# Kernel optimization log

Hardware: AMD Instinct MI355X
Metric: run time of the kernel (lower is better)

The kernel has to match this reference:

```python
import jax, jax.numpy as jnp
import numpy as np

LN_EPS = 1e-5
RMS_EPS = 1.1920929e-07  # torch.finfo(float32).eps (RMSNorm default eps=None)


def _layernorm(x, g, b):
    m = jnp.mean(x, axis=-1, keepdims=True)
    xc = x - m
    v = jnp.mean(xc * xc, axis=-1, keepdims=True)
    return xc / jnp.sqrt(v + LN_EPS) * g + b


def setup_inputs() -> dict:
    key = jax.random.key(0)
    ks = jax.random.split(key, 8)
    L, D, H, M, B, S = 4, 512, 8, 2048, 4, 2048
    std = 0.02
    return {
        "x": jax.random.normal(ks[0], (B, S, D), dtype=jnp.float32),
        # torch nn.Linear weights are [out, in]
        "Wq": jax.random.normal(ks[1], (L, D, D), dtype=jnp.float32) * std,
        "Wk": jax.random.normal(ks[2], (L, D, D), dtype=jnp.float32) * std,
        "Wv": jax.random.normal(ks[3], (L, D, D), dtype=jnp.float32) * std,
        "rms_w": jnp.ones((L, H, D // H), dtype=jnp.float32),
        "Wo": jax.random.normal(ks[4], (L, D, D), dtype=jnp.float32) * std,
        "bo": jnp.zeros((L, D), dtype=jnp.float32),
        "diffw": jnp.full((L,), 0.2, dtype=jnp.float32),
        "g_ffn": jnp.ones((L, D), dtype=jnp.float32),
        "b_ffn": jnp.zeros((L, D), dtype=jnp.float32),
        "W1": jax.random.normal(ks[5], (L, M, D), dtype=jnp.float32) * std,
        "b1": jnp.zeros((L, M), dtype=jnp.float32),
        "W2": jax.random.normal(ks[6], (L, D, M), dtype=jnp.float32) * std,
        "b2": jnp.zeros((L, D), dtype=jnp.float32),
        "g_f": jnp.ones((D,), dtype=jnp.float32),
        "b_f": jnp.zeros((D,), dtype=jnp.float32),
    }


def reference(x, Wq, Wk, Wv, rms_w, Wo, bo, diffw, g_ffn, b_ffn, W1, b1, W2, b2, g_f, b_f):
    def layer(xc, p):
        wq, wk, wv, rw, wo, bob, dw, g1, bn1, w1, bb1, w2, bb2 = p
        B, S, D = xc.shape
        H = rw.shape[0]
        F = D // (2 * H)  # per-component head dim (q/k split in two)
        qs = (xc @ wq.T).reshape(B, S, H, 2, F)
        ks_ = (xc @ wk.T).reshape(B, S, H, 2, F)
        scores = jnp.einsum('bqhif,bkhif->ibhqk', qs, ks_) * (F ** -0.5)
        atts = jax.nn.softmax(scores, axis=-1)  # [2,B,H,S,S]
        att = atts[0] - dw * atts[1]  # differential attention
        vs = (xc @ wv.T).reshape(B, S, H, D // H)
        o = jnp.einsum('bhqk,bkhe->bqhe', att, vs)  # [B,S,H,D/H]
        # fused per-token RMSNorm over (heads, head_dim)
        o = o / jnp.sqrt(jnp.mean(o * o, axis=(-2, -1), keepdims=True) + RMS_EPS) * rw
        xa = (o.reshape(B, S, D) @ wo.T + bob) * (1.0 - dw)
        xc = xa + xc  # attn residual
        h = _layernorm(xc, g1, bn1)
        h = jax.nn.gelu(h @ w1.T + bb1, approximate=False)
        xc = (h @ w2.T + bb2) + xc  # ffn residual
        return xc, None

    xf, _ = jax.lax.scan(layer, x, (Wq, Wk, Wv, rms_w, Wo, bo, diffw, g_ffn, b_ffn, W1, b1, W2, b2))
    return _layernorm(xf, g_f, b_f)
```

## Files before the change

kernel.cpp:

```cpp
#include <hip/hip_runtime.h>
#include <math.h>

#define B_ 4
#define S_ 2048
#define D_ 512
#define H_ 8
#define E_ 64
#define M_ 2048
#define L_ 4
#define R_ (B_ * S_)
#define RD_ ((size_t)R_ * D_)

typedef unsigned short u16;
typedef short short8 __attribute__((ext_vector_type(8)));
typedef short s16x4 __attribute__((ext_vector_type(4)));
typedef float f32x4 __attribute__((ext_vector_type(4)));

__device__ __forceinline__ float4 ldg4(const float* p) {
    return *reinterpret_cast<const float4*>(p);
}
__device__ __forceinline__ float gelu_f(float x) {
    return 0.5f * x * (1.0f + erff(x * 0.70710678118654752440f));
}
__device__ __forceinline__ unsigned int cvt_pk_bf16(float lo, float hi) {
    unsigned int r;
    asm("v_cvt_pk_bf16_f32 %0, %1, %2" : "=v"(r) : "v"(lo), "v"(hi));
    return r;
}
__device__ __forceinline__ float fast_exp2(float x) {
    return __builtin_amdgcn_exp2f(x);
}
__device__ __forceinline__ float bf2f(u16 u) {
    union { unsigned int i; float f; } v; v.i = ((unsigned int)u) << 16;
    return v.f;
}

#define LDT 40
template <int EPI, int TM>
__global__ __launch_bounds__(256) void gemm_bf16(
    const u16* __restrict__ A, const u16* __restrict__ W,
    const float* __restrict__ bias, const float* __restrict__ res,
    const float* __restrict__ dwp, float* __restrict__ Cf,
    u16* __restrict__ Cb, int M, int N, int K, int ldc)
{
    constexpr int BMv = TM * 32;
    __shared__ __align__(16) u16 As[2][BMv * LDT];
    __shared__ __align__(16) u16 Bs[2][128 * LDT];

    const int t  = threadIdx.x;
    const int w  = t >> 6, l = t & 63;
    const int lr = l & 15, lk8 = (l >> 4) << 3;
    const int wr = (w >> 1) * (TM * 16), wc = (w & 1) * 64;
    const int bm = blockIdx.x * BMv, bn = blockIdx.y * 128;

    int arow, acol;
    if constexpr (TM == 4) { arow = t >> 1; acol = (t & 1) << 4; }
    else                   { arow = t >> 2; acol = (t & 3) << 3; }
    const int brow = t >> 1, bcol = (t & 1) << 4;

    const u16* Ag = A + (size_t)(bm + arow) * K + acol;
    const u16* Wg = W + (size_t)(bn + brow) * K + bcol;

    f32x4 acc[TM][4];
#pragma unroll
    for (int m = 0; m < TM; ++m)
#pragma unroll
        for (int n = 0; n < 4; ++n) acc[m][n] = (f32x4){0.f, 0.f, 0.f, 0.f};

    constexpr int NA = (TM == 4) ? 2 : 1;
    short8 av[2], bv[2];
    av[0] = *reinterpret_cast<const short8*>(Ag);
    if (NA == 2) av[1] = *reinterpret_cast<const short8*>(Ag + 8);
    bv[0] = *reinterpret_cast<const short8*>(Wg);
    bv[1] = *reinterpret_cast<const short8*>(Wg + 8);

    const int sa = arow * LDT + acol;
    const int sb = brow * LDT + bcol;
    *reinterpret_cast<short8*>(&As[0][sa]) = av[0];
    if (NA == 2) *reinterpret_cast<short8*>(&As[0][sa + 8]) = av[1];
    *reinterpret_cast<short8*>(&Bs[0][sb]) = bv[0];
    *reinterpret_cast<short8*>(&Bs[0][sb + 8]) = bv[1];
    __syncthreads();

    const int NT = K >> 5;
    int cur = 0;
    for (int kt = 0; kt < NT; ++kt) {
        const bool pf = (kt + 1 < NT);
        if (pf) {
            const u16* An = Ag + ((kt + 1) << 5);
            const u16* Wn = Wg + ((kt + 1) << 5);
            av[0] = *reinterpret_cast<const short8*>(An);
            if (NA == 2) av[1] = *reinterpret_cast<const short8*>(An + 8);
            bv[0] = *reinterpret_cast<const short8*>(Wn);
            bv[1] = *reinterpret_cast<const short8*>(Wn + 8);
        }
        short8 af[TM], bfv[4];
#pragma unroll
        for (int m = 0; m < TM; ++m)
            af[m] = *reinterpret_cast<const short8*>(&As[cur][(wr + m * 16 + lr) * LDT + lk8]);
#pragma unroll
        for (int n = 0; n < 4; ++n)
            bfv[n] = *reinterpret_cast<const short8*>(&Bs[cur][(wc + n * 16 + lr) * LDT + lk8]);
#pragma unroll
        for (int m = 0; m < TM; ++m)
#pragma unroll
            for (int n = 0; n < 4; ++n)
                acc[m][n] = __builtin_amdgcn_mfma_f32_16x16x32_bf16(af[m], bfv[n], acc[m][n], 0, 0, 0);
        if (pf) {
            *reinterpret_cast<short8*>(&As[cur ^ 1][sa]) = av[0];
            if (NA == 2) *reinterpret_cast<short8*>(&As[cur ^ 1][sa + 8]) = av[1];
            *reinterpret_cast<short8*>(&Bs[cur ^ 1][sb]) = bv[0];
            *reinterpret_cast<short8*>(&Bs[cur ^ 1][sb + 8]) = bv[1];
        }
        __syncthreads();
        cur ^= 1;
    }

    float sc1 = 1.f;
    if constexpr (EPI == 1) sc1 = 1.f - dwp[0];
    float bcolv[4] = {0.f, 0.f, 0.f, 0.f};
    if constexpr (EPI >= 1) {
#pragma unroll
        for (int n = 0; n < 4; ++n) bcolv[n] = bias[bn + wc + n * 16 + lr];
    }
#pragma unroll
    for (int m = 0; m < TM; ++m) {
        const int row0 = bm + wr + m * 16 + (l >> 4) * 4;
#pragma unroll
        for (int n = 0; n < 4; ++n) {
            const int col = bn + wc + n * 16 + lr;
            float vv[4];
#pragma unroll
            for (int q = 0; q < 4; ++q) {
                const int row = row0 + q;
                float v = acc[m][n][q];
                if constexpr (EPI >= 1) v += bcolv[n];
                if constexpr (EPI == 1) v = v * sc1 + res[(size_t)row * N + col];
                if constexpr (EPI == 2) v = gelu_f(v);
                if constexpr (EPI == 3) v += res[(size_t)row * N + col];
                if constexpr (EPI == 1 || EPI == 3) Cf[(size_t)row * N + col] = v;
                vv[q] = v;
            }
            const unsigned int pa = cvt_pk_bf16(vv[0], vv[1]);
            const unsigned int pb = cvt_pk_bf16(vv[2], vv[3]);
            Cb[(size_t)(row0 + 0) * ldc + col] = (u16)pa;
            Cb[(size_t)(row0 + 1) * ldc + col] = (u16)(pa >> 16);
            Cb[(size_t)(row0 + 2) * ldc + col] = (u16)pb;
            Cb[(size_t)(row0 + 3) * ldc + col] = (u16)(pb >> 16);
        }
    }
}

#define LDSW 72
#define QKVLD 1536
__global__ __launch_bounds__(512) void attn_mfma(
    const u16* __restrict__ QKV, u16* __restrict__ O,
    const float* __restrict__ dwp)
{
    __shared__ __align__(16) u16 Ks[64][LDSW];
    __shared__ __align__(16) u16 Vt[64][LDSW];
    __shared__ __align__(16) u16 Ps[128][LDSW];

    const int t   = threadIdx.x;
    const int w   = t >> 6;
    const int l   = t & 63;
    const int lr  = l & 15;
    const int g   = l >> 4;
    const int lk8 = g << 3;

    const int d   = blockIdx.y * 16 + blockIdx.x;
    const int s   = d >> 3;
    const int bh  = (d & 7) * 4 + (s >> 4);
    const int qt  = s & 15;
    const int b   = bh >> 3, h = bh & 7;

    const float dw = dwp[0];
    const float C = 0.17677669529663687f * 1.44269504088896340736f;
    const size_t tokbase = (size_t)b * S_;

    const u16* qrow = QKV + (tokbase + (size_t)(qt * 128 + w * 16 + lr)) * QKVLD + h * E_;
    short8 qf[2];
    {
        short8 qr0 = *reinterpret_cast<const short8*>(qrow + lk8);
        short8 qr1 = *reinterpret_cast<const short8*>(qrow + 32 + lk8);
        uint4 u0, u1;
        u0.x = cvt_pk_bf16(bf2f((u16)qr0[0]) * C, bf2f((u16)qr0[1]) * C);
        u0.y = cvt_pk_bf16(bf2f((u16)qr0[2]) * C, bf2f((u16)qr0[3]) * C);
        u0.z = cvt_pk_bf16(bf2f((u16)qr0[4]) * C, bf2f((u16)qr0[5]) * C);
        u0.w = cvt_pk_bf16(bf2f((u16)qr0[6]) * C, bf2f((u16)qr0[7]) * C);
        u1.x = cvt_pk_bf16(bf2f((u16)qr1[0]) * C, bf2f((u16)qr1[1]) * C);
        u1.y = cvt_pk_bf16(bf2f((u16)qr1[2]) * C, bf2f((u16)qr1[3]) * C);
        u1.z = cvt_pk_bf16(bf2f((u16)qr1[4]) * C, bf2f((u16)qr1[5]) * C);
        u1.w = cvt_pk_bf16(bf2f((u16)qr1[6]) * C, bf2f((u16)qr1[7]) * C);
        qf[0] = *reinterpret_cast<short8*>(&u0);
        qf[1] = *reinterpret_cast<short8*>(&u1);
    }

    float lsum[2] = {0.f, 0.f};
    f32x4 oacc[2][4];
#pragma unroll
    for (int c = 0; c < 2; ++c)
#pragma unroll
        for (int et = 0; et < 4; ++et) oacc[c][et] = (f32x4){0.f, 0.f, 0.f, 0.f};

    const int sr   = t >> 3;
    const int sc0  = (t & 7) << 3;
    const int vswz = (sc0 >> 4) << 4;
    const int prow = w * 16 + lr;

    for (int kt = 0; kt < S_ / 64; ++kt) {
        const u16* kp = QKV + (tokbase + (size_t)(kt * 64 + sr)) * QKVLD + h * E_ + 512 + sc0;
        const u16* vp = kp + 512;
        short8 kv = *reinterpret_cast<const short8*>(kp);
        short8 vv = *reinterpret_cast<const short8*>(vp);
        __syncthreads();
        *reinterpret_cast<short8*>(&Ks[sr][sc0]) = kv;
        {
            const int vcol = sr ^ vswz;
#pragma unroll
            for (int i = 0; i < 8; ++i)
                Vt[sc0 + i][vcol] = (u16)vv[i];
        }
        __syncthreads();

#pragma unroll
        for (int c = 0; c < 2; ++c) {
            f32x4 sacc[4];
            const f32x4 zf = (f32x4){0.f, 0.f, 0.f, 0.f};
#pragma unroll
            for (int kc = 0; kc < 4; ++kc) {
                short8 kf = *reinterpret_cast<const short8*>(&Ks[kc * 16 + lr][c * 32 + lk8]);
                sacc[kc] = __builtin_amdgcn_mfma_f32_16x16x32_bf16(kf, qf[c], zf, 0, 0, 0);
            }
            float ls = 0.f;
#pragma unroll
            for (int kc = 0; kc < 4; ++kc) {
                float p0 = fast_exp2(sacc[kc][0]);
                float p1 = fast_exp2(sacc[kc][1]);
                float p2 = fast_exp2(sacc[kc][2]);
                float p3 = fast_exp2(sacc[kc][3]);
                ls += (p0 + p1) + (p2 + p3);
                uint2 pk;
                pk.x = cvt_pk_bf16(p0, p1);
                pk.y = cvt_pk_bf16(p2, p3);
                *reinterpret_cast<uint2*>(&Ps[prow][kc * 16 + (g << 2)]) = pk;
            }
            lsum[c] += ls;
            short8 pf0 = *reinterpret_cast<const short8*>(&Ps[prow][lk8]);
            short8 pf1 = *reinterpret_cast<const short8*>(&Ps[prow][32 + lk8]);
#pragma unroll
            for (int et = 0; et < 4; ++et) {
                short8 vf0 = *reinterpret_cast<const short8*>(&Vt[et * 16 + lr][(lk8) ^ (et << 4)]);
                short8 vf1 = *reinterpret_cast<const short8*>(&Vt[et * 16 + lr][(32 + lk8) ^ (et << 4)]);
                oacc[c][et] = __builtin_amdgcn_mfma_f32_16x16x32_bf16(vf0, pf0, oacc[c][et], 0, 0, 0);
                oacc[c][et] = __builtin_amdgcn_mfma_f32_16x16x32_bf16(vf1, pf1, oacc[c][et], 0, 0, 0);
            }
        }
    }

#pragma unroll
    for (int c = 0; c < 2; ++c) {
        lsum[c] += __shfl_xor(lsum[c], 16, 64);
        lsum[c] += __shfl_xor(lsum[c], 32, 64);
    }
    const float inv0 = 1.f / lsum[0];
    const float inv1 = dw / lsum[1];

    const size_t row = tokbase + (size_t)(qt * 128 + w * 16 + lr);
    u16* op = O + row * D_ + h * E_ + (g << 2);
#pragma unroll
    for (int et = 0; et < 4; ++et) {
        uint2 ov;
        ov.x = cvt_pk_bf16(oacc[0][et][0] * inv0 - oacc[1][et][0] * inv1,
                           oacc[0][et][1] * inv0 - oacc[1][et][1] * inv1);
        ov.y = cvt_pk_bf16(oacc[0][et][2] * inv0 - oacc[1][et][2] * inv1,
                           oacc[0][et][3] * inv0 - oacc[1][et][3] * inv1);
        *reinterpret_cast<uint2*>(op + et * 16) = ov;
    }
}

__global__ __launch_bounds__(256) void rmsnorm_bf(
    u16* __restrict__ X, const float* __restrict__ rw)
{
    const int row  = (blockIdx.x << 2) + (threadIdx.x >> 6);
    const int lane = threadIdx.x & 63;
    u16* xp = X + (size_t)row * D_ + lane * 8;
    short8 xv = *reinterpret_cast<const short8*>(xp);
    float xf[8];
#pragma unroll
    for (int i = 0; i < 8; ++i) xf[i] = bf2f((u16)xv[i]);
    float q = 0.f;
#pragma unroll
    for (int i = 0; i < 8; ++i) q += xf[i] * xf[i];
#pragma unroll
    for (int o = 1; o < 64; o <<= 1) q += __shfl_xor(q, o, 64);
    const float rstd = rsqrtf(q * (1.0f / 512.0f) + 1.1920929e-07f);
    const float* wp = rw + lane * 8;
    float4 w0 = ldg4(wp), w1 = ldg4(wp + 4);
    uint4 yv;
    yv.x = cvt_pk_bf16(xf[0] * rstd * w0.x, xf[1] * rstd * w0.y);
    yv.y = cvt_pk_bf16(xf[2] * rstd * w0.z, xf[3] * rstd * w0.w);
    yv.z = cvt_pk_bf16(xf[4] * rstd * w1.x, xf[5] * rstd * w1.y);
    yv.w = cvt_pk_bf16(xf[6] * rstd * w1.z, xf[7] * rstd * w1.w);
    *reinterpret_cast<uint4*>(xp) = yv;
}

template <int OUT>
__global__ __launch_bounds__(256) void layernorm_k(
    const float* __restrict__ X, const float* __restrict__ g,
    const float* __restrict__ bb, float* __restrict__ Yf,
    u16* __restrict__ Yb, float eps)
{
    const int row  = (blockIdx.x << 2) + (threadIdx.x >> 6);
    const int lane = threadIdx.x & 63;
    const float* xp = X + (size_t)row * D_;
    float4 x0 = ldg4(xp + lane * 4);
    float4 x1 = ldg4(xp + 256 + lane * 4);

    float s = x0.x + x0.y + x0.z + x0.w + x1.x + x1.y + x1.z + x1.w;
#pragma unroll
    for (int o = 1; o < 64; o <<= 1) s += __shfl_xor(s, o, 64);
    const float mean = s * (1.0f / 512.0f);

    x0.x -= mean; x0.y -= mean; x0.z -= mean; x0.w -= mean;
    x1.x -= mean; x1.y -= mean; x1.z -= mean; x1.w -= mean;
    float q = x0.x * x0.x + x0.y * x0.y + x0.z * x0.z + x0.w * x0.w
            + x1.x * x1.x + x1.y * x1.y + x1.z * x1.z + x1.w * x1.w;
#pragma unroll
    for (int o = 1; o < 64; o <<= 1) q += __shfl_xor(q, o, 64);
    const float rstd = rsqrtf(q * (1.0f / 512.0f) + eps);

    float4 g0 = ldg4(g + lane * 4),  g1 = ldg4(g + 256 + lane * 4);
    float4 b0 = ldg4(bb + lane * 4), b1 = ldg4(bb + 256 + lane * 4);
    float y[8];
    y[0] = x0.x * rstd * g0.x + b0.x; y[1] = x0.y * rstd * g0.y + b0.y;
    y[2] = x0.z * rstd * g0.z + b0.z; y[3] = x0.w * rstd * g0.w + b0.w;
    y[4] = x1.x * rstd * g1.x + b1.x; y[5] = x1.y * rstd * g1.y + b1.y;
    y[6] = x1.z * rstd * g1.z + b1.z; y[7] = x1.w * rstd * g1.w + b1.w;
    if constexpr (OUT == 0) {
        float* yp = Yf + (size_t)row * D_;
        *reinterpret_cast<float4*>(yp + lane * 4)       = make_float4(y[0], y[1], y[2], y[3]);
        *reinterpret_cast<float4*>(yp + 256 + lane * 4) = make_float4(y[4], y[5], y[6], y[7]);
    } else {
        u16* yp = Yb + (size_t)row * D_;
        uint2 a, b;
        a.x = cvt_pk_bf16(y[0], y[1]); a.y = cvt_pk_bf16(y[2], y[3]);
        b.x = cvt_pk_bf16(y[4], y[5]); b.y = cvt_pk_bf16(y[6], y[7]);
        *reinterpret_cast<uint2*>(yp + lane * 4)       = a;
        *reinterpret_cast<uint2*>(yp + 256 + lane * 4) = b;
    }
}

__global__ __launch_bounds__(256) void initcvt(
    const float* __restrict__ x, float* __restrict__ xc, u16* __restrict__ xcb)
{
    const size_t i = ((size_t)blockIdx.x * 256 + threadIdx.x) * 4;
    float4 v = ldg4(x + i);
    *reinterpret_cast<float4*>(xc + i) = v;
    uint2 o;
    o.x = cvt_pk_bf16(v.x, v.y); o.y = cvt_pk_bf16(v.z, v.w);
    *reinterpret_cast<uint2*>(xcb + i) = o;
}

__global__ __launch_bounds__(256) void conv_layer_w(
    const float* __restrict__ Wq, const float* __restrict__ Wk,
    const float* __restrict__ Wv, const float* __restrict__ Wo,
    const float* __restrict__ W1, const float* __restrict__ W2,
    u16* __restrict__ wqkv, u16* __restrict__ wo,
    u16* __restrict__ w1, u16* __restrict__ w2)
{
    const size_t i = ((size_t)blockIdx.x * 256 + threadIdx.x) * 4;
    const float* src; u16* dst;
    if (i < 786432) {
        dst = wqkv + i;
        if (i < 262144)      src = Wq + i;
        else if (i < 524288) src = Wk + (i - 262144);
        else                 src = Wv + (i - 524288);
    } else if (i < 1048576) { src = Wo + (i - 786432);  dst = wo + (i - 786432); }
    else if (i < 2097152)   { src = W1 + (i - 1048576); dst = w1 + (i - 1048576); }
    else                    { src = W2 + (i - 2097152); dst = w2 + (i - 2097152); }
    float4 v = ldg4(src);
    uint2 o;
    o.x = cvt_pk_bf16(v.x, v.y); o.y = cvt_pk_bf16(v.z, v.w);
    *reinterpret_cast<uint2*>(dst) = o;
}

extern "C" void kernel_launch(void* const* d_in, const int* in_sizes, int n_in,
                              void* d_out, int out_size, void* d_ws, size_t ws_size,
                              hipStream_t stream)
{
    const float* x     = (const float*)d_in[0];
    const float* Wq    = (const float*)d_in[1];
    const float* Wk    = (const float*)d_in[2];
    const float* Wv    = (const float*)d_in[3];
    const float* rms_w = (const float*)d_in[4];
    const float* Wo    = (const float*)d_in[5];
    const float* bo    = (const float*)d_in[6];
    const float* diffw = (const float*)d_in[7];
    const float* g_ffn = (const float*)d_in[8];
    const float* b_ffn = (const float*)d_in[9];
    const float* W1    = (const float*)d_in[10];
    const float* b1    = (const float*)d_in[11];
    const float* W2    = (const float*)d_in[12];
    const float* b2    = (const float*)d_in[13];
    const float* g_f   = (const float*)d_in[14];
    const float* b_f   = (const float*)d_in[15];

    char* ws = (char*)d_ws;
    float* xc   = (float*)(ws);
    u16*   xcb  = (u16*)(ws + 16777216);
    u16*   qkvb = (u16*)(ws + 25165824);
    u16*   ob   = (u16*)(ws + 50331648);
    u16*   tb   = qkvb;
    u16*   hb   = (u16*)(ws + 33554432);
    u16*   wqkv = (u16*)(ws + 67108864);
    u16*   wo_b = (u16*)(ws + 68681728);
    u16*   w1_b = (u16*)(ws + 69206016);
    u16*   w2_b = (u16*)(ws + 71303168);

    const dim3 blk(256);
    initcvt<<<dim3(RD_ / 4 / 256), blk, 0, stream>>>(x, xc, xcb);

    const dim3 g_tok(R_ / 4);

    for (int l = 0; l < L_; ++l) {
        const float* bo_l = bo + (size_t)l * D_;
        const float* b1_l = b1 + (size_t)l * M_;
        const float* b2_l = b2 + (size_t)l * D_;
        const float* dw_l = diffw + l;

        conv_layer_w<<<dim3(3072), blk, 0, stream>>>(
            Wq + (size_t)l * D_ * D_, Wk + (size_t)l * D_ * D_,
            Wv + (size_t)l * D_ * D_, Wo + (size_t)l * D_ * D_,
            W1 + (size_t)l * M_ * D_, W2 + (size_t)l * D_ * M_,
            wqkv, wo_b, w1_b, w2_b);

        gemm_bf16<0, 4><<<dim3(R_ / 128, 12), blk, 0, stream>>>(
            xcb, wqkv, nullptr, nullptr, nullptr, nullptr, qkvb,
            R_, 1536, D_, 1536);

        attn_mfma<<<dim3(S_ / 128, B_ * H_), dim3(512), 0, stream>>>(qkvb, ob, dw_l);

        rmsnorm_bf<<<g_tok, blk, 0, stream>>>(ob, rms_w + (size_t)l * D_);

        gemm_bf16<1, 2><<<dim3(R_ / 64, 4), blk, 0, stream>>>(
            ob, wo_b, bo_l, xc, dw_l, xc, xcb, R_, D_, D_, D_);

        layernorm_k<1><<<g_tok, blk, 0, stream>>>(
            xc, g_ffn + (size_t)l * D_, b_ffn + (size_t)l * D_, nullptr, tb, 1e-5f);

        gemm_bf16<2, 4><<<dim3(R_ / 128, 16), blk, 0, stream>>>(
            tb, w1_b, b1_l, nullptr, nullptr, nullptr, hb, R_, M_, D_, M_);

        gemm_bf16<3, 2><<<dim3(R_ / 64, 4), blk, 0, stream>>>(
            hb, w2_b, b2_l, xc, nullptr, xc, xcb, R_, D_, M_, D_);
    }

    layernorm_k<0><<<g_tok, blk, 0, stream>>>(xc, g_f, b_f, (float*)d_out, nullptr, 1e-5f);
}
```

Before: 847.9 us.

## Prefetch next K/V tile into registers and hoist V fragment loads in diff-attention

The attention loop now issues global loads for the next K/V tile before computing on the current one, then writes them to shared memory after the compute, so global-load latency overlaps the MFMA work. The V-transpose swizzle is changed to XOR the full column offset, with a matching read swizzle that depends on the row, to reduce LDS bank conflicts. V fragments are loaded once per tile and reused across both softmax components instead of being reloaded for each. This costs extra registers for the prefetched data and the hoisted fragments, which may lower occupancy.

```diff
diff --git a/kernel.cpp b/kernel.cpp
--- a/kernel.cpp
+++ b/kernel.cpp
@@ -13,7 +13,6 @@
 
 typedef unsigned short u16;
 typedef short short8 __attribute__((ext_vector_type(8)));
-typedef short s16x4 __attribute__((ext_vector_type(4)));
 typedef float f32x4 __attribute__((ext_vector_type(4)));
 
 __device__ __forceinline__ float4 ldg4(const float* p) {
@@ -205,23 +204,40 @@
 
     const int sr   = t >> 3;
     const int sc0  = (t & 7) << 3;
-    const int vswz = (sc0 >> 4) << 4;
     const int prow = w * 16 + lr;
-
-    for (int kt = 0; kt < S_ / 64; ++kt) {
-        const u16* kp = QKV + (tokbase + (size_t)(kt * 64 + sr)) * QKVLD + h * E_ + 512 + sc0;
-        const u16* vp = kp + 512;
+    const int vbit = lr & 8;
+
+    const u16* kbase = QKV + tokbase * QKVLD + h * E_ + 512 + sc0;
+
+    {
+        const u16* kp = kbase + (size_t)sr * QKVLD;
         short8 kv = *reinterpret_cast<const short8*>(kp);
-        short8 vv = *reinterpret_cast<const short8*>(vp);
-        __syncthreads();
+        short8 vv = *reinterpret_cast<const short8*>(kp + 512);
         *reinterpret_cast<short8*>(&Ks[sr][sc0]) = kv;
-        {
-            const int vcol = sr ^ vswz;
-#pragma unroll
-            for (int i = 0; i < 8; ++i)
-                Vt[sc0 + i][vcol] = (u16)vv[i];
-        }
-        __syncthreads();
+        const int vcol = sr ^ sc0;
+#pragma unroll
+        for (int i = 0; i < 8; ++i)
+            Vt[sc0 + i][vcol] = (u16)vv[i];
+    }
+    __syncthreads();
+
+    const int NT = S_ / 64;
+    short8 kv_n, vv_n;
+    for (int kt = 0; kt < NT; ++kt) {
+        const bool pf = (kt + 1 < NT);
+        if (pf) {
+            const u16* kp = kbase + (size_t)((kt + 1) * 64 + sr) * QKVLD;
+            kv_n = *reinterpret_cast<const short8*>(kp);
+            vv_n = *reinterpret_cast<const short8*>(kp + 512);
+        }
+
+        short8 vfr[4][2];
+#pragma unroll
+        for (int et = 0; et < 4; ++et) {
+            const int vx = (et << 4) ^ vbit;
+            vfr[et][0] = *reinterpret_cast<const short8*>(&Vt[et * 16 + lr][lk8 ^ vx]);
+            vfr[et][1] = *reinterpret_cast<const short8*>(&Vt[et * 16 + lr][(32 + lk8) ^ vx]);
+        }
 
 #pragma unroll
         for (int c = 0; c < 2; ++c) {
@@ -250,11 +266,19 @@
             short8 pf1 = *reinterpret_cast<const short8*>(&Ps[prow][32 + lk8]);
 #pragma unroll
             for (int et = 0; et < 4; ++et) {
-                short8 vf0 = *reinterpret_cast<const short8*>(&Vt[et * 16 + lr][(lk8) ^ (et << 4)]);
-                short8 vf1 = *reinterpret_cast<const short8*>(&Vt[et * 16 + lr][(32 + lk8) ^ (et << 4)]);
-                oacc[c][et] = __builtin_amdgcn_mfma_f32_16x16x32_bf16(vf0, pf0, oacc[c][et], 0, 0, 0);
-                oacc[c][et] = __builtin_amdgcn_mfma_f32_16x16x32_bf16(vf1, pf1, oacc[c][et], 0, 0, 0);
+                oacc[c][et] = __builtin_amdgcn_mfma_f32_16x16x32_bf16(vfr[et][0], pf0, oacc[c][et], 0, 0, 0);
+                oacc[c][et] = __builtin_amdgcn_mfma_f32_16x16x32_bf16(vfr[et][1], pf1, oacc[c][et], 0, 0, 0);
             }
+        }
+
+        if (pf) {
+            __syncthreads();
+            *reinterpret_cast<short8*>(&Ks[sr][sc0]) = kv_n;
+            const int vcol = sr ^ sc0;
+#pragma unroll
+            for (int i = 0; i < 8; ++i)
+                Vt[sc0 + i][vcol] = (u16)vv_n[i];
+            __syncthreads();
         }
     }
 
```

New measurement: 802.6 us (median of 2 runs). 1.06x faster.
